# Kernel optimization log

Hardware: AMD Instinct MI355X
Metric: run time of the kernel (lower is better)

Reference implementation:

```python
import jax, jax.numpy as jnp
from jax import lax
import numpy as np

# static config (matches init_kwargs)
B, H, Wd, C = 32, 96, 96, 64
nW, K, PAD = 4, 3, 1
WS = 48  # window_size = H // sqrt(nW)


def setup_inputs() -> dict:
    key = jax.random.key(0)
    ks = jax.random.split(key, 24)
    def p(i, shape, s=0.02):
        return jax.random.normal(ks[i], shape, dtype=jnp.float32) * s
    return {
        "x": jax.random.normal(ks[0], (B, H * Wd, C), dtype=jnp.float32),
        # se: conv1x1 -> gelu -> conv1x1 -> sigmoid
        "se_w1": p(1, (C, C)), "se_b1": p(2, (C,)),
        "se_w2": p(3, (C, C)), "se_b2": p(4, (C,)),
        # WinKernel_Reweight
        "dc_w": p(5, (nW, C)), "dc_b": p(6, (nW,)),            # grouped 1x1, nW groups of C->1
        "l1_w": p(7, (4 * nW, nW)), "l1_b": p(8, (4 * nW,)),
        "l2_w": p(9, (nW, 4 * nW)), "l2_b": p(10, (nW,)),
        # gk_fusion: grouped 1x1 (dim groups, nW->1 per group)
        "gkf_w": p(11, (C, nW)), "gkf_b": p(12, (C,)),
        # Fusion (gk_sum)
        "fu_proj_w": p(13, (C, nW, nW)), "fu_proj_b": p(14, (C * nW,)),  # grouped 1x1, dim groups of nW->nW
        "fu_fc1_w": p(15, (C, nW * C)), "fu_fc1_b": p(16, (C,)),
        "fu_fc2_w": p(17, (nW * C, C)), "fu_fc2_b": p(18, (nW * C,)),
        "fu_po_w": p(19, (C, C)), "fu_po_b": p(20, (C,)),
        # final proj_out
        "po_w": p(21, (C, C)), "po_b": p(22, (C,)),
    }


def _gelu(t):
    return jax.nn.gelu(t, approximate=False)  # torch nn.GELU default = exact erf


def _conv1x1(w, b, t):
    return jnp.einsum('oi,bihw->bohw', w, t) + b[None, :, None, None]


def _forward(x, se_w1, se_b1, se_w2, se_b2, dc_w, dc_b, l1_w, l1_b, l2_w, l2_b,
             gkf_w, gkf_b, fu_proj_w, fu_proj_b, fu_fc1_w, fu_fc1_b,
             fu_fc2_w, fu_fc2_b, fu_po_w, fu_po_b, po_w, po_b):
    xh = x.reshape(B, H, Wd, C)
    # window_partition -> (B*nW, C, WS, WS), windows row-major within each batch element
    win = (xh.reshape(B, 2, WS, 2, WS, C)
             .transpose(0, 1, 3, 2, 4, 5)
             .reshape(B * nW, WS, WS, C)
             .transpose(0, 3, 1, 2))
    # adaptive avg pool (WS->K, exact since WS % K == 0)
    pool = WS // K
    kern = win.reshape(B * nW, C, K, pool, K, pool).mean(axis=(3, 5))  # (B*nW, C, K, K)
    # SE block replaces kernels
    kern_se = jax.nn.sigmoid(_conv1x1(se_w2, se_b2, _gelu(_conv1x1(se_w1, se_b1, kern))))
    # WinKernel_Reweight
    xwin = win.reshape(B, nW * C, WS, WS)
    ww = xwin.mean(axis=(2, 3)).reshape(B, nW, C)                 # GAP then grouped 1x1 (nW groups)
    ww = jnp.einsum('wc,bwc->bw', dc_w, ww) + dc_b                # (B, nW)
    ww = _gelu(ww @ l1_w.T + l1_b)
    ww = jax.nn.sigmoid(ww @ l2_w.T + l2_b)                       # (B, nW)
    kr = kern_se.reshape(B, nW, C, K, K) * ww[:, :, None, None, None]
    # gk_fusion: after transpose(1,2) channel order is c-major; grouped conv -> per-c mix over windows
    gkf = jnp.einsum('cw,bwcij->bcij', gkf_w, kr) + gkf_b[None, :, None, None]  # (B, C, K, K)
    # Fusion (gk_sum) on SE kernels (window-major channel layout)
    feats_in = kern_se.reshape(B, nW * C, K, K)
    fg = feats_in.reshape(B, C, nW, K, K)                         # groups = consecutive nW channels
    feats = _gelu(jnp.einsum('goi,bgikl->bgokl', fu_proj_w, fg)
                  + fu_proj_b.reshape(1, C, nW, 1, 1))
    v = feats.mean(axis=(3, 4)).reshape(B, C * nW)                # GAP
    v = _gelu(v @ fu_fc1_w.T + fu_fc1_b)                          # (B, C)
    av = jax.nn.softmax((v @ fu_fc2_w.T + fu_fc2_b).reshape(B, nW, C), axis=1)
    x_sum = jnp.einsum('bwckl,bwc->bckl', feats_in.reshape(B, nW, C, K, K), av)
    gks = gkf + _conv1x1(fu_po_w, fu_po_b, x_sum)                 # (B, C, K, K)
    # assemble per-(sample, kernel-branch, channel) depthwise kernels and convolve
    gk = jnp.stack([gkf, gks], axis=1).reshape(B * 2 * C, 1, K, K)
    xi = jnp.broadcast_to(xh.transpose(0, 3, 1, 2)[:, None], (B, 2, C, H, Wd))
    xi = xi.reshape(1, B * 2 * C, H, Wd)
    y = lax.conv_general_dilated(xi, gk, window_strides=(1, 1),
                                 padding=((PAD, PAD), (PAD, PAD)),
                                 feature_group_count=B * 2 * C,
                                 dimension_numbers=('NCHW', 'OIHW', 'NCHW'))
    y = y.reshape(B, 2, C, H, Wd).sum(axis=1)                     # sum the two kernel branches
    y = _conv1x1(po_w, po_b, y)
    return y.transpose(0, 2, 3, 1).reshape(B, H * Wd, C)


def reference(x, se_w1, se_b1, se_w2, se_b2, dc_w, dc_b, l1_w, l1_b, l2_w, l2_b,
              gkf_w, gkf_b, fu_proj_w, fu_proj_b, fu_fc1_w, fu_fc1_b,
              fu_fc2_w, fu_fc2_b, fu_po_w, fu_po_b, po_w, po_b):
    return _forward(x, se_w1, se_b1, se_w2, se_b2, dc_w, dc_b, l1_w, l1_b, l2_w, l2_b,
                    gkf_w, gkf_b, fu_proj_w, fu_proj_b, fu_fc1_w, fu_fc1_b,
                    fu_fc2_w, fu_fc2_b, fu_po_w, fu_po_b, po_w, po_b)
```

## Files before the change

### kernel.cpp

```cpp
#include <hip/hip_runtime.h>
#include <hip/hip_bf16.h>

#define NPIX 9216

typedef __attribute__((ext_vector_type(8))) short short8v;
typedef __attribute__((ext_vector_type(4))) float floatx4;

__device__ __forceinline__ float geluf(float x){
  return 0.5f * x * (1.0f + erff(x * 0.70710678118654752440f));
}
__device__ __forceinline__ float sigm(float x){
  return 1.0f / (1.0f + expf(-x));
}
__device__ __forceinline__ unsigned short f2bf(float f){
  __hip_bfloat16 h = __float2bfloat16(f);
  return *(unsigned short*)&h;
}

__global__ __launch_bounds__(256) void k_pool(const float* __restrict__ x,
                                              float* __restrict__ kern)
{
  int blk = blockIdx.x;
  int bw = blk / 9, rem = blk % 9;
  int ki = rem / 3, kj = rem % 3;
  int b = bw >> 2, w = bw & 3;
  int wr = w >> 1, wc = w & 1;
  int t = threadIdx.x;
  int cg = t & 15, rw = t >> 4;
  int h = wr*48 + ki*16 + rw;
  int col0 = wc*48 + kj*16;
  size_t base = ((size_t)(b*NPIX + h*96 + col0))*64 + cg*4;
  float a0=0.f,a1=0.f,a2=0.f,a3=0.f;
  #pragma unroll
  for (int j=0;j<16;j++){
    float4 u = *(const float4*)(x + base + (size_t)j*64);
    a0 += u.x; a1 += u.y; a2 += u.z; a3 += u.w;
  }
  __shared__ float red[16*64];
  float* rr = &red[rw*64 + cg*4];
  rr[0]=a0; rr[1]=a1; rr[2]=a2; rr[3]=a3;
  __syncthreads();
  if (t < 64){
    float s = 0.f;
    #pragma unroll
    for (int r=0;r<16;r++) s += red[r*64 + t];
    kern[(size_t)bw*576 + t*9 + rem] = s * (1.0f/256.0f);
  }
}

__global__ __launch_bounds__(256) void k_small(const float* __restrict__ kern_ws,
    const float* __restrict__ se_w1, const float* __restrict__ se_b1,
    const float* __restrict__ se_w2, const float* __restrict__ se_b2,
    const float* __restrict__ dc_w,  const float* __restrict__ dc_b,
    const float* __restrict__ l1_w,  const float* __restrict__ l1_b,
    const float* __restrict__ l2_w,  const float* __restrict__ l2_b,
    const float* __restrict__ gkf_w, const float* __restrict__ gkf_b,
    const float* __restrict__ fu_proj_w, const float* __restrict__ fu_proj_b,
    const float* __restrict__ fu_fc1_w,  const float* __restrict__ fu_fc1_b,
    const float* __restrict__ fu_fc2_w,  const float* __restrict__ fu_fc2_b,
    const float* __restrict__ fu_po_w,   const float* __restrict__ fu_po_b,
    const float* __restrict__ po_w,
    float* __restrict__ kc_ws,
    unsigned short* __restrict__ frag_pw)
{
  int b = blockIdx.x;
  int t = threadIdx.x;
  __shared__ float s_kern[4*64*9];
  __shared__ float s_w[4096];
  __shared__ float s_tmp[4*64*9];
  __shared__ float s_kse[4*64*9];
  __shared__ float s_wwc[256];
  __shared__ float s_small[64];
  __shared__ float s_gkf[576];
  __shared__ float s_v0[256];
  __shared__ float s_v1[64];
  __shared__ float s_av[256];
  __shared__ float s_xsum[576];

  if (b == 0){
    for (int idx=t; idx<4096; idx+=256){
      int f = idx >> 9, L = (idx >> 3) & 63, j = idx & 7;
      int nb = f >> 1, kb = f & 1;
      int o = nb*16 + (L & 15);
      int c = kb*32 + ((L >> 4) & 3)*8 + j;
      frag_pw[idx] = f2bf(po_w[o*64 + c]);
    }
  }

  for (int idx=t; idx<2304; idx+=256) s_kern[idx] = kern_ws[b*2304 + idx];
  for (int idx=t; idx<4096; idx+=256){ int o=idx>>6, i=idx&63; s_w[i*64+o] = se_w1[idx]; }
  __syncthreads();
  for (int idx=t; idx<2304; idx+=256){
    int w = idx/576, rem = idx%576, o = rem/9, p = rem%9;
    float acc = se_b1[o];
    const float* kcol = &s_kern[w*576 + p];
    #pragma unroll 8
    for (int i=0;i<64;i++) acc += s_w[i*64+o]*kcol[i*9];
    s_tmp[idx] = geluf(acc);
  }
  __syncthreads();
  for (int idx=t; idx<4096; idx+=256){ int o=idx>>6, i=idx&63; s_w[i*64+o] = se_w2[idx]; }
  __syncthreads();
  for (int idx=t; idx<2304; idx+=256){
    int w = idx/576, rem = idx%576, o = rem/9, p = rem%9;
    float acc = se_b2[o];
    const float* gcol = &s_tmp[w*576 + p];
    #pragma unroll 8
    for (int i=0;i<64;i++) acc += s_w[i*64+o]*gcol[i*9];
    s_kse[idx] = sigm(acc);
  }
  __syncthreads();
  { int w = t>>6, c = t&63; float s=0.f;
    #pragma unroll
    for (int p=0;p<9;p++) s += s_kern[w*576+c*9+p];
    s_wwc[t] = s*(1.0f/9.0f); }
  __syncthreads();
  if (t<4){ float acc = dc_b[t];
    for (int c=0;c<64;c++) acc += dc_w[t*64+c]*s_wwc[t*64+c];
    s_small[t]=acc; }
  __syncthreads();
  if (t<16){ float acc = l1_b[t];
    #pragma unroll
    for (int w=0;w<4;w++) acc += l1_w[t*4+w]*s_small[w];
    s_small[16+t]=geluf(acc); }
  __syncthreads();
  if (t<4){ float acc = l2_b[t];
    #pragma unroll
    for (int j=0;j<16;j++) acc += l2_w[t*16+j]*s_small[16+j];
    s_small[32+t]=sigm(acc); }
  __syncthreads();
  for (int idx=t; idx<576; idx+=256){
    int c = idx/9, p = idx%9;
    float acc = gkf_b[c];
    #pragma unroll
    for (int w=0;w<4;w++) acc += gkf_w[c*4+w]*s_kse[w*576+c*9+p]*s_small[32+w];
    s_gkf[idx] = acc;
  }
  for (int idx=t; idx<2304; idx+=256){
    int g = idx/36, rem = idx%36, o = rem/9, p = rem%9;
    float acc = fu_proj_b[g*4+o];
    #pragma unroll
    for (int i=0;i<4;i++){
      int ch = g*4+i;
      acc += fu_proj_w[(g*4+o)*4+i] * s_kse[(ch>>6)*576 + (ch&63)*9 + p];
    }
    s_tmp[idx] = geluf(acc);
  }
  __syncthreads();
  { float s=0.f;
    #pragma unroll
    for (int p=0;p<9;p++) s += s_tmp[t*9+p];
    s_v0[t] = s*(1.0f/9.0f); }
  __syncthreads();
  if (t<64){ float acc = fu_fc1_b[t];
    for (int k=0;k<256;k++) acc += fu_fc1_w[t*256+k]*s_v0[k];
    s_v1[t]=geluf(acc); }
  __syncthreads();
  { float acc = fu_fc2_b[t];
    #pragma unroll 8
    for (int o2=0;o2<64;o2++) acc += fu_fc2_w[t*64+o2]*s_v1[o2];
    s_av[t]=acc; }
  __syncthreads();
  if (t<64){
    float z0=s_av[t], z1=s_av[64+t], z2=s_av[128+t], z3=s_av[192+t];
    float mx = fmaxf(fmaxf(z0,z1),fmaxf(z2,z3));
    float e0=expf(z0-mx), e1=expf(z1-mx), e2=expf(z2-mx), e3=expf(z3-mx);
    float inv = 1.0f/(e0+e1+e2+e3);
    s_av[t]=e0*inv; s_av[64+t]=e1*inv; s_av[128+t]=e2*inv; s_av[192+t]=e3*inv;
  }
  __syncthreads();
  for (int idx=t; idx<576; idx+=256){
    int c=idx/9, p=idx%9; float s=0.f;
    #pragma unroll
    for (int w=0;w<4;w++) s += s_kse[w*576+c*9+p]*s_av[w*64+c];
    s_xsum[idx]=s;
  }
  __syncthreads();
  for (int idx=t; idx<576; idx+=256){
    int c=idx/9, p=idx%9;
    float acc = 2.0f*s_gkf[idx] + fu_po_b[c];
    #pragma unroll 8
    for (int i=0;i<64;i++) acc += fu_po_w[c*64+i]*s_xsum[i*9+p];
    kc_ws[b*576+idx] = acc;
  }
}

__global__ __launch_bounds__(256, 4) void k_conv(const float* __restrict__ x,
                                                 const float* __restrict__ kc_ws,
                                                 const unsigned short* __restrict__ frag_pw,
                                                 const float* __restrict__ po_b,
                                                 float* __restrict__ out)
{
  int bi = blockIdx.x;
  int b = bi / 144, tile = bi % 144;
  int th = tile / 12, tw = tile % 12;
  int h0 = th*8, w0 = tw*8;
  int t = threadIdx.x;

  __shared__ float s_x[100*64];
  __shared__ unsigned short s_tmp[64*72];
  __shared__ float s_kc[576];

  for (int idx=t; idx<1600; idx+=256){
    int pix = idx >> 4, c4 = idx & 15;
    int r = pix / 10, col = pix % 10;
    int hh = h0 - 1 + r, ww = w0 - 1 + col;
    float4 v = make_float4(0.f,0.f,0.f,0.f);
    if (hh >= 0 && hh < 96 && ww >= 0 && ww < 96)
      v = *(const float4*)(x + (((size_t)b*NPIX + hh*96 + ww)<<6) + c4*4);
    *(float4*)&s_x[pix*64 + c4*4] = v;
  }
  for (int idx=t; idx<576; idx+=256) s_kc[idx] = kc_ws[b*576 + idx];
  __syncthreads();

  {
    int c = t & 63, rg = t >> 6;
    int r0 = rg*2;
    float k0=s_kc[c*9+0],k1=s_kc[c*9+1],k2=s_kc[c*9+2],
          k3=s_kc[c*9+3],k4=s_kc[c*9+4],k5=s_kc[c*9+5],
          k6=s_kc[c*9+6],k7=s_kc[c*9+7],k8=s_kc[c*9+8];
    float row[4][10];
    #pragma unroll
    for (int rr=0; rr<4; rr++)
      #pragma unroll
      for (int cc=0; cc<10; cc++)
        row[rr][cc] = s_x[((r0+rr)*10 + cc)*64 + c];
    #pragma unroll
    for (int dr=0; dr<2; dr++){
      int pr = r0 + dr;
      #pragma unroll
      for (int pc=0; pc<8; pc++){
        float acc = k0*row[dr+0][pc] + k1*row[dr+0][pc+1] + k2*row[dr+0][pc+2]
                  + k3*row[dr+1][pc] + k4*row[dr+1][pc+1] + k5*row[dr+1][pc+2]
                  + k6*row[dr+2][pc] + k7*row[dr+2][pc+1] + k8*row[dr+2][pc+2];
        s_tmp[(pr*8 + pc)*72 + c] = f2bf(acc);
      }
    }
  }
  __syncthreads();

  {
    int wv = t >> 6, lane = t & 63;
    int m = wv*16 + (lane & 15);
    int quad = lane >> 4;
    floatx4 acc[4] = {{0.f,0.f,0.f,0.f},{0.f,0.f,0.f,0.f},
                      {0.f,0.f,0.f,0.f},{0.f,0.f,0.f,0.f}};
    #pragma unroll
    for (int kb=0; kb<2; kb++){
      short8v afrag = *(const short8v*)&s_tmp[m*72 + kb*32 + quad*8];
      #pragma unroll
      for (int nb=0; nb<4; nb++){
        short8v bfrag = *(const short8v*)(frag_pw + (nb*2+kb)*512 + lane*8);
        acc[nb] = __builtin_amdgcn_mfma_f32_16x16x32_bf16(afrag, bfrag, acc[nb], 0, 0, 0);
      }
    }
    #pragma unroll
    for (int nb=0; nb<4; nb++){
      int o = nb*16 + (lane & 15);
      float pb = po_b[o];
      #pragma unroll
      for (int r=0; r<4; r++){
        int px = wv*16 + quad*4 + r;
        int hh = h0 + (px >> 3), wwp = w0 + (px & 7);
        out[(((size_t)b*NPIX + hh*96 + wwp)<<6) + o] = acc[nb][r] + pb;
      }
    }
  }
}

extern "C" void kernel_launch(void* const* d_in, const int* in_sizes, int n_in,
                              void* d_out, int out_size, void* d_ws, size_t ws_size,
                              hipStream_t stream) {
  const float* x        = (const float*)d_in[0];
  const float* se_w1    = (const float*)d_in[1];
  const float* se_b1    = (const float*)d_in[2];
  const float* se_w2    = (const float*)d_in[3];
  const float* se_b2    = (const float*)d_in[4];
  const float* dc_w     = (const float*)d_in[5];
  const float* dc_b     = (const float*)d_in[6];
  const float* l1_w     = (const float*)d_in[7];
  const float* l1_b     = (const float*)d_in[8];
  const float* l2_w     = (const float*)d_in[9];
  const float* l2_b     = (const float*)d_in[10];
  const float* gkf_w    = (const float*)d_in[11];
  const float* gkf_b    = (const float*)d_in[12];
  const float* fu_proj_w= (const float*)d_in[13];
  const float* fu_proj_b= (const float*)d_in[14];
  const float* fu_fc1_w = (const float*)d_in[15];
  const float* fu_fc1_b = (const float*)d_in[16];
  const float* fu_fc2_w = (const float*)d_in[17];
  const float* fu_fc2_b = (const float*)d_in[18];
  const float* fu_po_w  = (const float*)d_in[19];
  const float* fu_po_b  = (const float*)d_in[20];
  const float* po_w     = (const float*)d_in[21];
  const float* po_b     = (const float*)d_in[22];

  float* kern_ws = (float*)d_ws;
  float* kc_ws   = kern_ws + 73728;
  unsigned short* frag_pw = (unsigned short*)(kc_ws + 18432);

  k_pool<<<1152, 256, 0, stream>>>(x, kern_ws);
  k_small<<<32, 256, 0, stream>>>(kern_ws, se_w1, se_b1, se_w2, se_b2,
                                  dc_w, dc_b, l1_w, l1_b, l2_w, l2_b,
                                  gkf_w, gkf_b, fu_proj_w, fu_proj_b,
                                  fu_fc1_w, fu_fc1_b, fu_fc2_w, fu_fc2_b,
                                  fu_po_w, fu_po_b, po_w, kc_ws, frag_pw);
  k_conv<<<4608, 256, 0, stream>>>(x, kc_ws, frag_pw, po_b, (float*)d_out);
}
```

Baseline: 242.2 us.

## Restructure per-sample small-MLP kernel with padded LDS layouts and wave reductions

Rewrites the k_small kernel so each thread computes nine spatial outputs of the SE convolutions with vectorized float4 LDS reads, using padded (stride 12 and 65) shared layouts to avoid bank conflicts. Weight matrices for fu_proj and fu_po are staged in shared memory instead of being read repeatedly from global memory. The fc1/fc2 matvecs become coalesced wave-wide dot products reduced with shuffles, and index mappings are changed so consecutive threads touch consecutive channels. This targets the serialized, poorly coalesced small-kernel stage, at the cost of more shared memory and register pressure. The large conv kernel is unchanged, so the overall effect is limited by this stage's share of total time.

```diff
diff --git a/kernel.cpp b/kernel.cpp
--- a/kernel.cpp
+++ b/kernel.cpp
@@ -65,17 +65,20 @@
 {
   int b = blockIdx.x;
   int t = threadIdx.x;
-  __shared__ float s_kern[4*64*9];
-  __shared__ float s_w[4096];
-  __shared__ float s_tmp[4*64*9];
-  __shared__ float s_kse[4*64*9];
+  int lane = t & 63, wv = t >> 6;
+
+  __shared__ float s_kern[4*64*12];
+  __shared__ float s_t2[4*64*12];
+  __shared__ float s_w[64*65];
+  __shared__ float s_kse[2304];
+  __shared__ float s_feats[2304];
+  __shared__ float s_gkf[576];
+  __shared__ float s_xsum[576];
   __shared__ float s_wwc[256];
+  __shared__ float s_v0[256];
+  __shared__ float s_av[256];
+  __shared__ float s_v1[64];
   __shared__ float s_small[64];
-  __shared__ float s_gkf[576];
-  __shared__ float s_v0[256];
-  __shared__ float s_v1[64];
-  __shared__ float s_av[256];
-  __shared__ float s_xsum[576];
 
   if (b == 0){
     for (int idx=t; idx<4096; idx+=256){
@@ -87,34 +90,61 @@
     }
   }
 
-  for (int idx=t; idx<2304; idx+=256) s_kern[idx] = kern_ws[b*2304 + idx];
-  for (int idx=t; idx<4096; idx+=256){ int o=idx>>6, i=idx&63; s_w[i*64+o] = se_w1[idx]; }
-  __syncthreads();
   for (int idx=t; idx<2304; idx+=256){
-    int w = idx/576, rem = idx%576, o = rem/9, p = rem%9;
-    float acc = se_b1[o];
-    const float* kcol = &s_kern[w*576 + p];
+    int w = idx/576, rem = idx%576, c = rem/9, p = rem%9;
+    s_kern[(w*64+c)*12 + p] = kern_ws[b*2304 + idx];
+  }
+  for (int j=t; j<4096; j+=256){ int o=j>>6, i=j&63; s_w[i*65+o] = se_w1[j]; }
+  __syncthreads();
+
+  {
+    float bo = se_b1[lane];
+    float a0=bo,a1=bo,a2=bo,a3=bo,a4=bo,a5=bo,a6=bo,a7=bo,a8=bo;
     #pragma unroll 8
-    for (int i=0;i<64;i++) acc += s_w[i*64+o]*kcol[i*9];
-    s_tmp[idx] = geluf(acc);
-  }
-  __syncthreads();
-  for (int idx=t; idx<4096; idx+=256){ int o=idx>>6, i=idx&63; s_w[i*64+o] = se_w2[idx]; }
-  __syncthreads();
-  for (int idx=t; idx<2304; idx+=256){
-    int w = idx/576, rem = idx%576, o = rem/9, p = rem%9;
-    float acc = se_b2[o];
-    const float* gcol = &s_tmp[w*576 + p];
+    for (int i=0;i<64;i++){
+      float wvv = s_w[i*65 + lane];
+      const float* kr = &s_kern[(wv*64+i)*12];
+      float4 kA = *(const float4*)kr;
+      float4 kB = *(const float4*)(kr+4);
+      float kC = kr[8];
+      a0 += wvv*kA.x; a1 += wvv*kA.y; a2 += wvv*kA.z; a3 += wvv*kA.w;
+      a4 += wvv*kB.x; a5 += wvv*kB.y; a6 += wvv*kB.z; a7 += wvv*kB.w;
+      a8 += wvv*kC;
+    }
+    float* dst = &s_t2[(wv*64+lane)*12];
+    dst[0]=geluf(a0); dst[1]=geluf(a1); dst[2]=geluf(a2); dst[3]=geluf(a3);
+    dst[4]=geluf(a4); dst[5]=geluf(a5); dst[6]=geluf(a6); dst[7]=geluf(a7);
+    dst[8]=geluf(a8);
+  }
+  __syncthreads();
+
+  for (int j=t; j<4096; j+=256){ int o=j>>6, i=j&63; s_w[i*65+o] = se_w2[j]; }
+  __syncthreads();
+
+  {
+    float bo = se_b2[lane];
+    float a0=bo,a1=bo,a2=bo,a3=bo,a4=bo,a5=bo,a6=bo,a7=bo,a8=bo;
     #pragma unroll 8
-    for (int i=0;i<64;i++) acc += s_w[i*64+o]*gcol[i*9];
-    s_kse[idx] = sigm(acc);
-  }
-  __syncthreads();
-  { int w = t>>6, c = t&63; float s=0.f;
-    #pragma unroll
-    for (int p=0;p<9;p++) s += s_kern[w*576+c*9+p];
-    s_wwc[t] = s*(1.0f/9.0f); }
-  __syncthreads();
+    for (int i=0;i<64;i++){
+      float wvv = s_w[i*65 + lane];
+      const float* kr = &s_t2[(wv*64+i)*12];
+      float4 kA = *(const float4*)kr;
+      float4 kB = *(const float4*)(kr+4);
+      float kC = kr[8];
+      a0 += wvv*kA.x; a1 += wvv*kA.y; a2 += wvv*kA.z; a3 += wvv*kA.w;
+      a4 += wvv*kB.x; a5 += wvv*kB.y; a6 += wvv*kB.z; a7 += wvv*kB.w;
+      a8 += wvv*kC;
+    }
+    float* dst = &s_kse[wv*576 + lane*9];
+    dst[0]=sigm(a0); dst[1]=sigm(a1); dst[2]=sigm(a2); dst[3]=sigm(a3);
+    dst[4]=sigm(a4); dst[5]=sigm(a5); dst[6]=sigm(a6); dst[7]=sigm(a7);
+    dst[8]=sigm(a8);
+    const float* kr = &s_kern[(wv*64+lane)*12];
+    float s = kr[0]+kr[1]+kr[2]+kr[3]+kr[4]+kr[5]+kr[6]+kr[7]+kr[8];
+    s_wwc[wv*64+lane] = s * (1.0f/9.0f);
+  }
+  __syncthreads();
+
   if (t<4){ float acc = dc_b[t];
     for (int c=0;c<64;c++) acc += dc_w[t*64+c]*s_wwc[t*64+c];
     s_small[t]=acc; }
@@ -129,38 +159,65 @@
     for (int j=0;j<16;j++) acc += l2_w[t*16+j]*s_small[16+j];
     s_small[32+t]=sigm(acc); }
   __syncthreads();
+
+  for (int j=t; j<1024; j+=256){
+    int g = j>>4, oi = j&15;
+    s_w[g*17 + oi] = fu_proj_w[j];
+  }
   for (int idx=t; idx<576; idx+=256){
-    int c = idx/9, p = idx%9;
+    int c = idx & 63, p = idx >> 6;
     float acc = gkf_b[c];
     #pragma unroll
     for (int w=0;w<4;w++) acc += gkf_w[c*4+w]*s_kse[w*576+c*9+p]*s_small[32+w];
-    s_gkf[idx] = acc;
-  }
+    s_gkf[c*9+p] = acc;
+  }
+  __syncthreads();
+
   for (int idx=t; idx<2304; idx+=256){
-    int g = idx/36, rem = idx%36, o = rem/9, p = rem%9;
+    int g = idx & 63, op = idx >> 6;
+    int o = op / 9, p = op % 9;
     float acc = fu_proj_b[g*4+o];
     #pragma unroll
     for (int i=0;i<4;i++){
       int ch = g*4+i;
-      acc += fu_proj_w[(g*4+o)*4+i] * s_kse[(ch>>6)*576 + (ch&63)*9 + p];
-    }
-    s_tmp[idx] = geluf(acc);
-  }
-  __syncthreads();
+      acc += s_w[g*17 + o*4 + i] * s_kse[(ch>>6)*576 + (ch&63)*9 + p];
+    }
+    s_feats[(g*4+o)*9 + p] = geluf(acc);
+  }
+  __syncthreads();
+
   { float s=0.f;
     #pragma unroll
-    for (int p=0;p<9;p++) s += s_tmp[t*9+p];
+    for (int p=0;p<9;p++) s += s_feats[t*9+p];
     s_v0[t] = s*(1.0f/9.0f); }
   __syncthreads();
-  if (t<64){ float acc = fu_fc1_b[t];
-    for (int k=0;k<256;k++) acc += fu_fc1_w[t*256+k]*s_v0[k];
-    s_v1[t]=geluf(acc); }
-  __syncthreads();
-  { float acc = fu_fc2_b[t];
-    #pragma unroll 8
-    for (int o2=0;o2<64;o2++) acc += fu_fc2_w[t*64+o2]*s_v1[o2];
-    s_av[t]=acc; }
-  __syncthreads();
+
+  {
+    #pragma unroll
+    for (int oi=0; oi<16; oi++){
+      int o = wv*16 + oi;
+      float v = 0.f;
+      #pragma unroll
+      for (int kb=0; kb<4; kb++)
+        v += fu_fc1_w[o*256 + kb*64 + lane] * s_v0[kb*64 + lane];
+      #pragma unroll
+      for (int m=32; m>0; m>>=1) v += __shfl_xor(v, m);
+      if (lane == 0) s_v1[o] = geluf(v + fu_fc1_b[o]);
+    }
+  }
+  __syncthreads();
+
+  {
+    for (int mi=0; mi<64; mi++){
+      int m = wv*64 + mi;
+      float v = fu_fc2_w[m*64 + lane] * s_v1[lane];
+      #pragma unroll
+      for (int mm=32; mm>0; mm>>=1) v += __shfl_xor(v, mm);
+      if (lane == 0) s_av[m] = v + fu_fc2_b[m];
+    }
+  }
+  __syncthreads();
+
   if (t<64){
     float z0=s_av[t], z1=s_av[64+t], z2=s_av[128+t], z3=s_av[192+t];
     float mx = fmaxf(fmaxf(z0,z1),fmaxf(z2,z3));
@@ -169,19 +226,23 @@
     s_av[t]=e0*inv; s_av[64+t]=e1*inv; s_av[128+t]=e2*inv; s_av[192+t]=e3*inv;
   }
   __syncthreads();
+
+  for (int j=t; j<4096; j+=256){ int c=j>>6, i=j&63; s_w[i*65+c] = fu_po_w[j]; }
   for (int idx=t; idx<576; idx+=256){
-    int c=idx/9, p=idx%9; float s=0.f;
+    int c = idx & 63, p = idx >> 6;
+    float s=0.f;
     #pragma unroll
     for (int w=0;w<4;w++) s += s_kse[w*576+c*9+p]*s_av[w*64+c];
-    s_xsum[idx]=s;
-  }
-  __syncthreads();
+    s_xsum[c*9+p]=s;
+  }
+  __syncthreads();
+
   for (int idx=t; idx<576; idx+=256){
-    int c=idx/9, p=idx%9;
-    float acc = 2.0f*s_gkf[idx] + fu_po_b[c];
+    int c = idx & 63, p = idx >> 6;
+    float acc = 2.0f*s_gkf[c*9+p] + fu_po_b[c];
     #pragma unroll 8
-    for (int i=0;i<64;i++) acc += fu_po_w[c*64+i]*s_xsum[i*9+p];
-    kc_ws[b*576+idx] = acc;
+    for (int i=0;i<64;i++) acc += s_w[i*65+c]*s_xsum[i*9+p];
+    kc_ws[b*576 + c*9 + p] = acc;
   }
 }
 
```

Result: slower. 269.0 us (+11.1%).
